# Optimization experiments

Hardware: AMD Instinct MI355X
Metric: run time of the kernel (lower is better)

Reference implementation:

```python
import jax, jax.numpy as jnp
import numpy as np

B, N, D = 8, 4096, 512
H, RANK = 8, 64
HD = D // H


def _xavier(key, shape):
    fan_out, fan_in = shape
    limit = (6.0 / (fan_in + fan_out)) ** 0.5
    return jax.random.uniform(key, shape, jnp.float32, -limit, limit)


def setup_inputs() -> dict:
    key = jax.random.key(0)
    ks = jax.random.split(key, 10)
    return {
        "x": jax.random.normal(ks[0], (B, N, D), jnp.float32),
        "graph_bias": jax.random.normal(ks[1], (N, N), jnp.float32),
        # torch nn.Linear weight convention: (out_features, in_features)
        "w_qd": _xavier(ks[2], (RANK, D)),
        "w_qu": _xavier(ks[3], (D, RANK)),
        "w_kd": _xavier(ks[4], (RANK, D)),
        "w_ku": _xavier(ks[5], (D, RANK)),
        "w_vd": _xavier(ks[6], (RANK, D)),
        "w_vu": _xavier(ks[7], (D, RANK)),
        "w_od": _xavier(ks[8], (RANK, D)),
        "w_ou": _xavier(ks[9], (D, RANK)),
    }


def _feature_map(x):
    # ELU + 1 (ensures non-negativity for linear attention)
    return jax.nn.elu(x) + 1.0


def _heads(t):
    # (B, N, D) -> (B, H, N, HD)
    return t.reshape(B, N, H, HD).transpose(0, 2, 1, 3)


def reference(x, graph_bias, w_qd, w_qu, w_kd, w_ku, w_vd, w_vu, w_od, w_ou):
    # low-rank QKV projections (Linear has no bias): x @ W_down.T @ W_up.T
    Q = (x @ w_qd.T) @ w_qu.T
    K = (x @ w_kd.T) @ w_ku.T
    V = (x @ w_vd.T) @ w_vu.T
    Q = _feature_map(_heads(Q))
    K = _feature_map(_heads(K))
    V = _heads(V)

    # linear attention: phi(Q) (phi(K)^T V), O(N)
    KV = jnp.einsum('bhnd,bhnD->bhdD', K, V)
    out = jnp.einsum('bhnd,bhdD->bhnD', Q, KV)
    K_sum = K.sum(axis=2)                                   # (B,H,HD)
    normalizer = jnp.einsum('bhnd,bhd->bhn', Q, K_sum)      # (B,H,N)
    normalizer = jnp.clip(normalizer, 1e-6, None)
    out = out / normalizer[..., None]

    # graph-bias branch: dense softmax attention over learned structure
    bias_attn = jax.nn.softmax(graph_bias, axis=-1)         # (N,N)
    V_flat = V.transpose(0, 2, 1, 3).reshape(B, N, D)
    bias_out = jnp.einsum('ij,bjd->bid', bias_attn, V_flat)
    bias_out = _heads(bias_out)
    out = out + 0.1 * bias_out

    out = out.transpose(0, 2, 1, 3).reshape(B, N, D)
    out = (out @ w_od.T) @ w_ou.T
    return out
```

## Files before the change

kernel.cpp:

```cpp
#include <hip/hip_runtime.h>

typedef unsigned short u16;
typedef __attribute__((ext_vector_type(8))) short short8;
typedef __attribute__((ext_vector_type(4))) float f32x4;

#define GLD16(g, l) __builtin_amdgcn_global_load_lds((const __attribute__((address_space(1))) void*)(g), (__attribute__((address_space(3))) void*)(l), 16, 0, 0)

__device__ __forceinline__ u16 f2bf(float f){
  unsigned x = __float_as_uint(f);
  return (u16)((x + 0x7FFFu + ((x >> 16) & 1u)) >> 16);
}
__device__ __forceinline__ float bf2f(u16 u){
  return __uint_as_float(((unsigned)u) << 16);
}

__global__ __launch_bounds__(256) void castf2b(const float* __restrict__ src, u16* __restrict__ dst){
  const size_t i = ((size_t)blockIdx.x * 256 + threadIdx.x) * 8;
  float4 a = *reinterpret_cast<const float4*>(src + i);
  float4 b = *reinterpret_cast<const float4*>(src + i + 4);
  ushort4 o0 = {f2bf(a.x), f2bf(a.y), f2bf(a.z), f2bf(a.w)};
  ushort4 o1 = {f2bf(b.x), f2bf(b.y), f2bf(b.z), f2bf(b.w)};
  *reinterpret_cast<ushort4*>(dst + i) = o0;
  *reinterpret_cast<ushort4*>(dst + i + 4) = o1;
}

__global__ __launch_bounds__(256) void cast_pad(const float* __restrict__ src, u16* __restrict__ dst){
  const int i = blockIdx.x * 256 + threadIdx.x;
  const int e = i * 8;
  const int r = e >> 9;
  ushort4 o0 = {0,0,0,0}, o1 = {0,0,0,0};
  if(r < 64){
    float4 a = *reinterpret_cast<const float4*>(src + e);
    float4 b = *reinterpret_cast<const float4*>(src + e + 4);
    o0 = ushort4{f2bf(a.x), f2bf(a.y), f2bf(a.z), f2bf(a.w)};
    o1 = ushort4{f2bf(b.x), f2bf(b.y), f2bf(b.z), f2bf(b.w)};
  }
  *reinterpret_cast<ushort4*>(dst + e) = o0;
  *reinterpret_cast<ushort4*>(dst + e + 4) = o1;
}

__global__ __launch_bounds__(256) void softmax_rows(const float* __restrict__ gb,
                                                    u16* __restrict__ attn){
  const int row = blockIdx.x;
  const float* rp = gb + (size_t)row * 4096;
  u16* op = attn + (size_t)row * 4096;
  const int t = threadIdx.x;
  float4 v[4];
  float mx = -3.4e38f;
#pragma unroll
  for(int k = 0; k < 4; k++){
    v[k] = *reinterpret_cast<const float4*>(rp + k*1024 + t*4);
    mx = fmaxf(mx, fmaxf(fmaxf(v[k].x, v[k].y), fmaxf(v[k].z, v[k].w)));
  }
#pragma unroll
  for(int off = 32; off > 0; off >>= 1) mx = fmaxf(mx, __shfl_xor(mx, off, 64));
  __shared__ float sred[4];
  __shared__ float sred2[4];
  const int wid = t >> 6, lane = t & 63;
  if(lane == 0) sred[wid] = mx;
  __syncthreads();
  mx = fmaxf(fmaxf(sred[0], sred[1]), fmaxf(sred[2], sred[3]));
  float s = 0.f;
#pragma unroll
  for(int k = 0; k < 4; k++){
    v[k].x = __expf(v[k].x - mx); v[k].y = __expf(v[k].y - mx);
    v[k].z = __expf(v[k].z - mx); v[k].w = __expf(v[k].w - mx);
    s += v[k].x + v[k].y + v[k].z + v[k].w;
  }
#pragma unroll
  for(int off = 32; off > 0; off >>= 1) s += __shfl_xor(s, off, 64);
  if(lane == 0) sred2[wid] = s;
  __syncthreads();
  s = sred2[0] + sred2[1] + sred2[2] + sred2[3];
  const float inv = 1.f / s;
#pragma unroll
  for(int k = 0; k < 4; k++){
    ushort4 o;
    o.x = f2bf(v[k].x * inv); o.y = f2bf(v[k].y * inv);
    o.z = f2bf(v[k].z * inv); o.w = f2bf(v[k].w * inv);
    *reinterpret_cast<ushort4*>(op + k*1024 + t*4) = o;
  }
}

__global__ __launch_bounds__(256) void combine_w(const float* __restrict__ wu,
                                                 const float* __restrict__ wd,
                                                 u16* __restrict__ dst){
  __shared__ float au[64][68];
  __shared__ float bd[64][68];
  const int t = threadIdx.x;
  const int o0 = blockIdx.x << 6, i0 = blockIdx.y << 6;
#pragma unroll
  for(int q = 0; q < 4; q++){
    const int row = (q << 4) + (t >> 4);
    const int c4  = (t & 15) << 2;
    float4 u = *reinterpret_cast<const float4*>(wu + (size_t)(o0 + row) * 64 + c4);
    au[c4+0][row] = u.x; au[c4+1][row] = u.y; au[c4+2][row] = u.z; au[c4+3][row] = u.w;
    float4 v = *reinterpret_cast<const float4*>(wd + (size_t)row * 512 + i0 + c4);
    bd[row][c4+0] = v.x; bd[row][c4+1] = v.y; bd[row][c4+2] = v.z; bd[row][c4+3] = v.w;
  }
  __syncthreads();
  const int tr = t >> 4, tc = t & 15;
  float acc[4][4] = {};
#pragma unroll
  for(int kk = 0; kk < 64; kk++){
    const float4 a4 = *reinterpret_cast<const float4*>(&au[kk][tr << 2]);
    const float4 b4 = *reinterpret_cast<const float4*>(&bd[kk][tc << 2]);
    const float av_[4] = {a4.x, a4.y, a4.z, a4.w};
    const float bv_[4] = {b4.x, b4.y, b4.z, b4.w};
#pragma unroll
    for(int i = 0; i < 4; i++)
#pragma unroll
      for(int j = 0; j < 4; j++) acc[i][j] = fmaf(av_[i], bv_[j], acc[i][j]);
  }
#pragma unroll
  for(int i = 0; i < 4; i++){
    ushort4 o;
    o.x = f2bf(acc[i][0]); o.y = f2bf(acc[i][1]); o.z = f2bf(acc[i][2]); o.w = f2bf(acc[i][3]);
    *reinterpret_cast<ushort4*>(dst + (size_t)(o0 + (tr << 2) + i) * 512 + i0 + (tc << 2)) = o;
  }
}

__global__ __launch_bounds__(256) void wvo_kernel(const float* __restrict__ w_od,
                                                  const float* __restrict__ w_vu,
                                                  float* __restrict__ Wvo){
  __shared__ float As[16][68];
  __shared__ float Bs[16][68];
  const int t = threadIdx.x;
  const int tr = t >> 4, tc = t & 15;
  float acc[4][4] = {};
  for(int k0 = 0; k0 < 512; k0 += 16){
    __syncthreads();
#pragma unroll
    for(int q = 0; q < 4; q++){
      const int idx = q * 256 + t;
      const int kk = idx >> 6, l = idx & 63;
      As[kk][l] = w_od[(size_t)l * 512 + k0 + kk];
      Bs[kk][l] = w_vu[(size_t)(k0 + kk) * 64 + l];
    }
    __syncthreads();
#pragma unroll
    for(int kk = 0; kk < 16; kk++){
      const float4 a4 = *reinterpret_cast<const float4*>(&As[kk][tr << 2]);
      const float4 b4 = *reinterpret_cast<const float4*>(&Bs[kk][tc << 2]);
      const float av_[4] = {a4.x, a4.y, a4.z, a4.w};
      const float bv_[4] = {b4.x, b4.y, b4.z, b4.w};
#pragma unroll
      for(int i = 0; i < 4; i++)
#pragma unroll
        for(int j = 0; j < 4; j++) acc[i][j] = fmaf(av_[i], bv_[j], acc[i][j]);
    }
  }
#pragma unroll
  for(int i = 0; i < 4; i++)
#pragma unroll
    for(int j = 0; j < 4; j++)
      Wvo[(size_t)((tr << 2) + i) * 64 + (tc << 2) + j] = 0.1f * acc[i][j];
}

__global__ __launch_bounds__(256) void qkvlow_gemm(const u16* __restrict__ Am, const u16* __restrict__ Bm,
                                                   u16* __restrict__ Qt, u16* __restrict__ Kt,
                                                   u16* __restrict__ Vlowt, float* __restrict__ Ksum){
  __shared__ u16 As[128 * 32];
  __shared__ u16 Bs[128 * 32];
  const int t = threadIdx.x;
  const int wid = t >> 6, lane = t & 63;
  const int wr = wid >> 1, wc = wid & 1;
  const int bm = blockIdx.x << 7, bn = blockIdx.y << 7;
  f32x4 acc[4][4];
#pragma unroll
  for(int m = 0; m < 4; m++)
#pragma unroll
    for(int n = 0; n < 4; n++) acc[m][n] = f32x4{0.f, 0.f, 0.f, 0.f};
  const int frow = lane & 15;
  const int kg8  = (lane >> 4) << 3;
  const int c0 = t, c1 = t + 256;
  for(int k0 = 0; k0 < 512; k0 += 32){
    GLD16(Am + (size_t)(bm + (c0 >> 2)) * 512 + k0 + ((c0 & 3) << 3), ((char*)As) + (wid << 10));
    GLD16(Am + (size_t)(bm + (c1 >> 2)) * 512 + k0 + ((c1 & 3) << 3), ((char*)As) + 4096 + (wid << 10));
    GLD16(Bm + (size_t)(bn + (c0 >> 2)) * 512 + k0 + ((c0 & 3) << 3), ((char*)Bs) + (wid << 10));
    GLD16(Bm + (size_t)(bn + (c1 >> 2)) * 512 + k0 + ((c1 & 3) << 3), ((char*)Bs) + 4096 + (wid << 10));
    __syncthreads();
    short8 af[4], bfr[4];
#pragma unroll
    for(int m = 0; m < 4; m++){
      af[m]  = *reinterpret_cast<const short8*>(As + (((wr << 6) + (m << 4) + frow) << 5) + kg8);
      bfr[m] = *reinterpret_cast<const short8*>(Bs + (((wc << 6) + (m << 4) + frow) << 5) + kg8);
    }
#pragma unroll
    for(int m = 0; m < 4; m++)
#pragma unroll
      for(int n = 0; n < 4; n++)
        acc[m][n] = __builtin_amdgcn_mfma_f32_16x16x32_bf16(af[m], bfr[n], acc[m][n], 0, 0, 0);
    __syncthreads();
  }
  const int cn = lane & 15, rb4 = (lane >> 4) << 2;
  const int b = bm >> 12;
#pragma unroll
  for(int nf = 0; nf < 4; nf++){
    const int col = bn + (wc << 6) + (nf << 4) + cn;
    u16* rowp;
    bool isK = false, isQorK = false;
    if(col < 512){
      rowp = Qt + ((((size_t)((b << 3) + (col >> 6)) << 6) + (col & 63)) << 12);
      isQorK = true;
    } else if(col < 1024){
      const int c = col - 512;
      rowp = Kt + ((((size_t)((b << 3) + (c >> 6)) << 6) + (c & 63)) << 12);
      isK = true; isQorK = true;
    } else {
      const int j = col - 1024;
      if(j >= 64) continue;
      rowp = Vlowt + ((size_t)((b << 6) + j) << 12);
    }
    float ks = 0.f;
#pragma unroll
    for(int mf = 0; mf < 4; mf++){
      const int nn0 = (bm & 4095) + (wr << 6) + (mf << 4) + rb4;
      float v0 = acc[mf][nf][0], v1 = acc[mf][nf][1], v2 = acc[mf][nf][2], v3 = acc[mf][nf][3];
      if(isQorK){
        v0 = v0 > 0.f ? v0 + 1.f : __expf(v0);
        v1 = v1 > 0.f ? v1 + 1.f : __expf(v1);
        v2 = v2 > 0.f ? v2 + 1.f : __expf(v2);
        v3 = v3 > 0.f ? v3 + 1.f : __expf(v3);
      }
      if(isK) ks += v0 + v1 + v2 + v3;
      ushort4 o = {f2bf(v0), f2bf(v1), f2bf(v2), f2bf(v3)};
      *reinterpret_cast<ushort4*>(rowp + nn0) = o;
    }
    if(isK){
      ks += __shfl_xor(ks, 16);
      ks += __shfl_xor(ks, 32);
      if(lane < 16){
        const int c = col - 512;
        atomicAdd(Ksum + ((size_t)((b << 3) + (c >> 6)) << 6) + (c & 63), ks);
      }
    }
  }
}

__global__ __launch_bounds__(256) void kvlow_gemm(const u16* __restrict__ Kt,
                                                  const u16* __restrict__ Vlowt,
                                                  float* __restrict__ KVlow){
  __shared__ u16 As[64 * 32];
  __shared__ u16 Bs[64 * 32];
  const int bh = blockIdx.x, sp = blockIdx.y;
  const int b = bh >> 3;
  const int t = threadIdx.x;
  const int wid = t >> 6, lane = t & 63;
  const int frow = lane & 15, kg8 = (lane >> 4) << 3;
  const size_t kbase = (size_t)bh << 18;
  const size_t vbase = (size_t)b << 18;
  const int srow = t >> 2, soff = (t & 3) << 3;
  f32x4 acc[4];
#pragma unroll
  for(int n = 0; n < 4; n++) acc[n] = f32x4{0.f, 0.f, 0.f, 0.f};
  const int nend = (sp << 10) + 1024;
  for(int n0 = sp << 10; n0 < nend; n0 += 32){
    GLD16(Kt    + kbase + ((size_t)srow << 12) + n0 + soff, ((char*)As) + (wid << 10));
    GLD16(Vlowt + vbase + ((size_t)srow << 12) + n0 + soff, ((char*)Bs) + (wid << 10));
    __syncthreads();
    short8 af = *reinterpret_cast<const short8*>(As + (((wid << 4) + frow) << 5) + kg8);
#pragma unroll
    for(int n = 0; n < 4; n++){
      short8 bf8 = *reinterpret_cast<const short8*>(Bs + (((n << 4) + frow) << 5) + kg8);
      acc[n] = __builtin_amdgcn_mfma_f32_16x16x32_bf16(af, bf8, acc[n], 0, 0, 0);
    }
    __syncthreads();
  }
  const int cn = lane & 15, rb4 = (lane >> 4) << 2;
#pragma unroll
  for(int n = 0; n < 4; n++)
#pragma unroll
    for(int j = 0; j < 4; j++){
      const int d = (wid << 4) + rb4 + j;
      const int jj = (n << 4) + cn;
      atomicAdd(KVlow + ((size_t)bh << 12) + (size_t)d * 64 + jj, acc[n][j]);
    }
}

__global__ __launch_bounds__(256) void kv_apply(const float* __restrict__ KVlow,
                                                const float* __restrict__ w_vu,
                                                float* __restrict__ KVt){
  __shared__ float Kl[64][68];
  __shared__ float Wl[64][68];
  const int bh = blockIdx.x, h = bh & 7;
  const int t = threadIdx.x;
#pragma unroll
  for(int q = 0; q < 4; q++){
    const int row = (q << 4) + (t >> 4);
    const int c4  = (t & 15) << 2;
    float4 v = *reinterpret_cast<const float4*>(KVlow + ((size_t)bh << 12) + (size_t)row * 64 + c4);
    Kl[c4+0][row] = v.x; Kl[c4+1][row] = v.y; Kl[c4+2][row] = v.z; Kl[c4+3][row] = v.w;
    float4 w = *reinterpret_cast<const float4*>(w_vu + (size_t)((h << 6) + row) * 64 + c4);
    Wl[c4+0][row] = w.x; Wl[c4+1][row] = w.y; Wl[c4+2][row] = w.z; Wl[c4+3][row] = w.w;
  }
  __syncthreads();
  const int tr = t >> 4, tc = t & 15;
  float acc[4][4] = {};
#pragma unroll
  for(int kk = 0; kk < 64; kk++){
    const float4 a4 = *reinterpret_cast<const float4*>(&Wl[kk][tr << 2]);
    const float4 b4 = *reinterpret_cast<const float4*>(&Kl[kk][tc << 2]);
    const float av_[4] = {a4.x, a4.y, a4.z, a4.w};
    const float bv_[4] = {b4.x, b4.y, b4.z, b4.w};
#pragma unroll
    for(int i = 0; i < 4; i++)
#pragma unroll
      for(int j = 0; j < 4; j++) acc[i][j] = fmaf(av_[i], bv_[j], acc[i][j]);
  }
#pragma unroll
  for(int i = 0; i < 4; i++){
    float4 o = {acc[i][0], acc[i][1], acc[i][2], acc[i][3]};
    *reinterpret_cast<float4*>(KVt + ((size_t)bh << 12) + (size_t)((tr << 2) + i) * 64 + (tc << 2)) = o;
  }
}

__global__ __launch_bounds__(256) void bias_pv(const u16* __restrict__ Am,
                                               const u16* __restrict__ Bm,
                                               float* __restrict__ Pv){
  __shared__ u16 As[128 * 32];
  __shared__ u16 Bs[128 * 32];
  const int t = threadIdx.x;
  const int wid = t >> 6, lane = t & 63;
  const int wr = wid >> 1, wc = wid & 1;
  const int bm = blockIdx.x << 7, bn = blockIdx.y << 7, kz = blockIdx.z;
  f32x4 acc[4][4];
#pragma unroll
  for(int m = 0; m < 4; m++)
#pragma unroll
    for(int n = 0; n < 4; n++) acc[m][n] = f32x4{0.f, 0.f, 0.f, 0.f};
  const int frow = lane & 15;
  const int kg8  = (lane >> 4) << 3;
  const int c0 = t, c1 = t + 256;
  const int kend = (kz << 11) + 2048;
  for(int k0 = kz << 11; k0 < kend; k0 += 32){
    GLD16(Am + ((size_t)(bm + (c0 >> 2)) << 12) + k0 + ((c0 & 3) << 3), ((char*)As) + (wid << 10));
    GLD16(Am + ((size_t)(bm + (c1 >> 2)) << 12) + k0 + ((c1 & 3) << 3), ((char*)As) + 4096 + (wid << 10));
    GLD16(Bm + ((size_t)(bn + (c0 >> 2)) << 12) + k0 + ((c0 & 3) << 3), ((char*)Bs) + (wid << 10));
    GLD16(Bm + ((size_t)(bn + (c1 >> 2)) << 12) + k0 + ((c1 & 3) << 3), ((char*)Bs) + 4096 + (wid << 10));
    __syncthreads();
    short8 af[4], bfr[4];
#pragma unroll
    for(int m = 0; m < 4; m++){
      af[m]  = *reinterpret_cast<const short8*>(As + (((wr << 6) + (m << 4) + frow) << 5) + kg8);
      bfr[m] = *reinterpret_cast<const short8*>(Bs + (((wc << 6) + (m << 4) + frow) << 5) + kg8);
    }
#pragma unroll
    for(int m = 0; m < 4; m++)
#pragma unroll
      for(int n = 0; n < 4; n++)
        acc[m][n] = __builtin_amdgcn_mfma_f32_16x16x32_bf16(af[m], bfr[n], acc[m][n], 0, 0, 0);
    __syncthreads();
  }
  const int cn = lane & 15, rb4 = (lane >> 4) << 2;
  float* P = Pv + (size_t)kz * 2097152;
#pragma unroll
  for(int m = 0; m < 4; m++){
    const int row0 = bm + (wr << 6) + (m << 4) + rb4;
#pragma unroll
    for(int n = 0; n < 4; n++){
      const int col = bn + (wc << 6) + (n << 4) + cn;
#pragma unroll
      for(int j = 0; j < 4; j++)
        P[(size_t)(row0 + j) * 512 + col] = acc[m][n][j];
    }
  }
}

__global__ __launch_bounds__(256) void linattn(const u16* __restrict__ Qt,
                                               const float* __restrict__ KVt,
                                               const float* __restrict__ Ksum,
                                               u16* __restrict__ midb){
  __shared__ float qs[64][64];
  __shared__ float kvs[64][64];
  __shared__ float nrm[64];
  __shared__ float ksl[64];
  const int nblk = blockIdx.x, bhi = blockIdx.y;
  const int b = bhi >> 3, h = bhi & 7;
  const int n0 = nblk << 6;
  const int t = threadIdx.x;
#pragma unroll
  for(int q = 0; q < 4; q++){
    const int row = (q << 4) + (t >> 4);
    const int c4  = (t & 15) << 2;
    ushort4 u = *reinterpret_cast<const ushort4*>(Qt + ((((size_t)bhi << 6) + row) << 12) + n0 + c4);
    qs[row][c4+0] = bf2f(u.x); qs[row][c4+1] = bf2f(u.y); qs[row][c4+2] = bf2f(u.z); qs[row][c4+3] = bf2f(u.w);
    float4 v = *reinterpret_cast<const float4*>(KVt + ((size_t)bhi << 12) + (row << 6) + c4);
    kvs[c4+0][row] = v.x; kvs[c4+1][row] = v.y; kvs[c4+2][row] = v.z; kvs[c4+3][row] = v.w;
  }
  if(t < 64) ksl[t] = Ksum[((size_t)bhi << 6) + t];
  __syncthreads();
  if(t < 64){
    float s = 0.f;
    for(int d = 0; d < 64; d++) s = fmaf(qs[d][t], ksl[d], s);
    nrm[t] = fmaxf(s, 1e-6f);
  }
  __syncthreads();
  const int tr = t >> 4, tc = t & 15;
  float acc[4][4] = {};
#pragma unroll
  for(int kk = 0; kk < 64; kk++){
    const float4 a4 = *reinterpret_cast<const float4*>(&qs[kk][tr << 2]);
    const float4 b4 = *reinterpret_cast<const float4*>(&kvs[kk][tc << 2]);
    const float av_[4] = {a4.x, a4.y, a4.z, a4.w};
    const float bv_[4] = {b4.x, b4.y, b4.z, b4.w};
#pragma unroll
    for(int i = 0; i < 4; i++)
#pragma unroll
      for(int j = 0; j < 4; j++) acc[i][j] = fmaf(av_[i], bv_[j], acc[i][j]);
  }
#pragma unroll
  for(int i = 0; i < 4; i++){
    const int gn = n0 + (tr << 2) + i;
    const float inv = 1.f / nrm[(tr << 2) + i];
    const size_t oi = (((size_t)b << 12) + gn) * 512 + h * 64 + (tc << 2);
    ushort4 o = {f2bf(acc[i][0] * inv), f2bf(acc[i][1] * inv),
                 f2bf(acc[i][2] * inv), f2bf(acc[i][3] * inv)};
    *reinterpret_cast<ushort4*>(midb + oi) = o;
  }
}

__global__ __launch_bounds__(256) void biaslow(const float* __restrict__ Pv,
                                               const float* __restrict__ Wvo,
                                               float* __restrict__ G){
  __shared__ float Pl[64][68];
  __shared__ float Wl[64][68];
  const int nt = blockIdx.x, b = blockIdx.y;
  const int n0 = nt << 6;
  const int t = threadIdx.x;
#pragma unroll
  for(int q = 0; q < 4; q++){
    const int row = (q << 4) + (t >> 4);
    const int c4  = (t & 15) << 2;
    float4 v  = *reinterpret_cast<const float4*>(Pv + (size_t)(n0 + row) * 512 + (b << 6) + c4);
    float4 v2 = *reinterpret_cast<const float4*>(Pv + 2097152 + (size_t)(n0 + row) * 512 + (b << 6) + c4);
    Pl[c4+0][row] = v.x + v2.x; Pl[c4+1][row] = v.y + v2.y;
    Pl[c4+2][row] = v.z + v2.z; Pl[c4+3][row] = v.w + v2.w;
    float4 w = *reinterpret_cast<const float4*>(Wvo + (size_t)row * 64 + c4);
    Wl[c4+0][row] = w.x; Wl[c4+1][row] = w.y; Wl[c4+2][row] = w.z; Wl[c4+3][row] = w.w;
  }
  __syncthreads();
  const int tr = t >> 4, tc = t & 15;
  float acc[4][4] = {};
#pragma unroll
  for(int kk = 0; kk < 64; kk++){
    const float4 a4 = *reinterpret_cast<const float4*>(&Pl[kk][tr << 2]);
    const float4 b4 = *reinterpret_cast<const float4*>(&Wl[kk][tc << 2]);
    const float av_[4] = {a4.x, a4.y, a4.z, a4.w};
    const float bv_[4] = {b4.x, b4.y, b4.z, b4.w};
#pragma unroll
    for(int i = 0; i < 4; i++)
#pragma unroll
      for(int j = 0; j < 4; j++) acc[i][j] = fmaf(av_[i], bv_[j], acc[i][j]);
  }
#pragma unroll
  for(int i = 0; i < 4; i++){
    float4 o = {acc[i][0], acc[i][1], acc[i][2], acc[i][3]};
    *reinterpret_cast<float4*>(G + (size_t)(((size_t)b << 12) + n0 + (tr << 2) + i) * 64 + (tc << 2)) = o;
  }
}

__global__ __launch_bounds__(256) void down_gemm(const u16* __restrict__ Am,
                                                 const u16* __restrict__ Bw,
                                                 const float* __restrict__ Gin,
                                                 u16* __restrict__ Gb){
  __shared__ u16 As[128 * 32];
  const int t = threadIdx.x;
  const int wid = t >> 6, lane = t & 63;
  const int bm = blockIdx.x << 7;
  const int frow = lane & 15, kg8 = (lane >> 4) << 3;
  f32x4 acc[2][4];
#pragma unroll
  for(int m = 0; m < 2; m++)
#pragma unroll
    for(int n = 0; n < 4; n++) acc[m][n] = f32x4{0.f, 0.f, 0.f, 0.f};
  const int c0 = t, c1 = t + 256;
  for(int k0 = 0; k0 < 512; k0 += 32){
    GLD16(Am + (size_t)(bm + (c0 >> 2)) * 512 + k0 + ((c0 & 3) << 3), ((char*)As) + (wid << 10));
    GLD16(Am + (size_t)(bm + (c1 >> 2)) * 512 + k0 + ((c1 & 3) << 3), ((char*)As) + 4096 + (wid << 10));
    __syncthreads();
    short8 af[2], bfr[4];
#pragma unroll
    for(int m = 0; m < 2; m++)
      af[m] = *reinterpret_cast<const short8*>(As + (((wid << 5) + (m << 4) + frow) << 5) + kg8);
#pragma unroll
    for(int n = 0; n < 4; n++)
      bfr[n] = *reinterpret_cast<const short8*>(Bw + (size_t)((n << 4) + frow) * 512 + k0 + kg8);
#pragma unroll
    for(int m = 0; m < 2; m++)
#pragma unroll
      for(int n = 0; n < 4; n++)
        acc[m][n] = __builtin_amdgcn_mfma_f32_16x16x32_bf16(af[m], bfr[n], acc[m][n], 0, 0, 0);
    __syncthreads();
  }
  const int cn = lane & 15, rb4 = (lane >> 4) << 2;
#pragma unroll
  for(int m = 0; m < 2; m++){
#pragma unroll
    for(int n = 0; n < 4; n++){
      const int col = (n << 4) + cn;
#pragma unroll
      for(int j = 0; j < 4; j++){
        const int r = bm + (wid << 5) + (m << 4) + rb4 + j;
        const float v = acc[m][n][j] + Gin[(size_t)r * 64 + col];
        Gb[(size_t)r * 64 + col] = f2bf(v);
      }
    }
  }
}

__global__ __launch_bounds__(256) void up_gemm(const u16* __restrict__ Am,
                                               const u16* __restrict__ Bw,
                                               float* __restrict__ C){
  const int t = threadIdx.x;
  const int wid = t >> 6, lane = t & 63;
  const int wr = wid >> 1, wc = wid & 1;
  const int bm = blockIdx.x << 7, bn = blockIdx.y << 7;
  const int frow = lane & 15, kg8 = (lane >> 4) << 3;
  f32x4 acc[4][4];
#pragma unroll
  for(int m = 0; m < 4; m++)
#pragma unroll
    for(int n = 0; n < 4; n++) acc[m][n] = f32x4{0.f, 0.f, 0.f, 0.f};
  short8 af[4][2], bfr[4][2];
#pragma unroll
  for(int m = 0; m < 4; m++)
#pragma unroll
    for(int kk = 0; kk < 2; kk++)
      af[m][kk] = *reinterpret_cast<const short8*>(Am + (size_t)(bm + (wr << 6) + (m << 4) + frow) * 64 + (kk << 5) + kg8);
#pragma unroll
  for(int n = 0; n < 4; n++)
#pragma unroll
    for(int kk = 0; kk < 2; kk++)
      bfr[n][kk] = *reinterpret_cast<const short8*>(Bw + (size_t)(bn + (wc << 6) + (n << 4) + frow) * 64 + (kk << 5) + kg8);
#pragma unroll
  for(int m = 0; m < 4; m++)
#pragma unroll
    for(int n = 0; n < 4; n++){
      acc[m][n] = __builtin_amdgcn_mfma_f32_16x16x32_bf16(af[m][0], bfr[n][0], acc[m][n], 0, 0, 0);
      acc[m][n] = __builtin_amdgcn_mfma_f32_16x16x32_bf16(af[m][1], bfr[n][1], acc[m][n], 0, 0, 0);
    }
  const int cn = lane & 15, rb4 = (lane >> 4) << 2;
#pragma unroll
  for(int m = 0; m < 4; m++){
    const int row0 = bm + (wr << 6) + (m << 4) + rb4;
#pragma unroll
    for(int n = 0; n < 4; n++){
      const int col = bn + (wc << 6) + (n << 4) + cn;
#pragma unroll
      for(int j = 0; j < 4; j++)
        C[(size_t)(row0 + j) * 512 + col] = acc[m][n][j];
    }
  }
}

extern "C" void kernel_launch(void* const* d_in, const int* in_sizes, int n_in,
                              void* d_out, int out_size, void* d_ws, size_t ws_size,
                              hipStream_t stream){
  const float* x    = (const float*)d_in[0];
  const float* gb   = (const float*)d_in[1];
  const float* w_qd = (const float*)d_in[2];
  const float* w_qu = (const float*)d_in[3];
  const float* w_kd = (const float*)d_in[4];
  const float* w_ku = (const float*)d_in[5];
  const float* w_vd = (const float*)d_in[6];
  const float* w_vu = (const float*)d_in[7];
  const float* w_od = (const float*)d_in[8];
  const float* w_ou = (const float*)d_in[9];
  float* out = (float*)d_out;
  char* ws = (char*)d_ws;

  u16*   xb    = (u16*)  (ws);
  u16*   Kt    = (u16*)  (ws + 33554432);
  u16*   Wall  = (u16*)  (ws + 67108864);
  u16*   wodb  = (u16*)  (ws + 68288512);
  u16*   woub  = (u16*)  (ws + 68354048);
  float* Wvo   = (float*)(ws + 68419584);
  u16*   Qt    = (u16*)  (ws + 68435968);
  u16*   Vlowt = (u16*)  (ws + 101990400);
  u16*   attn  = (u16*)  (ws + 106184704);
  float* Pv    = (float*)(ws + 139739136);
  float* KVlow = (float*)(ws + 156516352);
  float* KVt   = (float*)(ws + 157564928);
  float* Ksum  = (float*)(ws + 158613504);
  u16*   midb  = (u16*)  (ws);
  float* G     = (float*)(ws + 33554432);
  u16*   Gb    = (u16*)  (ws + 41943040);

  hipMemsetAsync(KVlow, 0, 2113536, stream);

  combine_w<<<dim3(8, 8), 256, 0, stream>>>(w_qu, w_qd, Wall);
  combine_w<<<dim3(8, 8), 256, 0, stream>>>(w_ku, w_kd, Wall + 262144);
  cast_pad<<<32, 256, 0, stream>>>(w_vd, Wall + 524288);
  castf2b<<<16, 256, 0, stream>>>(w_od, wodb);
  castf2b<<<16, 256, 0, stream>>>(w_ou, woub);
  wvo_kernel<<<1, 256, 0, stream>>>(w_od, w_vu, Wvo);

  castf2b<<<8192, 256, 0, stream>>>(x, xb);
  softmax_rows<<<4096, 256, 0, stream>>>(gb, attn);

  qkvlow_gemm<<<dim3(256, 9), 256, 0, stream>>>(xb, Wall, Qt, Kt, Vlowt, Ksum);

  kvlow_gemm<<<dim3(64, 4), 256, 0, stream>>>(Kt, Vlowt, KVlow);
  kv_apply<<<64, 256, 0, stream>>>(KVlow, w_vu, KVt);

  bias_pv<<<dim3(32, 4, 2), 256, 0, stream>>>(attn, Vlowt, Pv);

  linattn<<<dim3(64, 64), 256, 0, stream>>>(Qt, KVt, Ksum, midb);

  biaslow<<<dim3(64, 8), 256, 0, stream>>>(Pv, Wvo, G);

  down_gemm<<<256, 256, 0, stream>>>(midb, wodb, G, Gb);

  up_gemm<<<dim3(256, 4), 256, 0, stream>>>(Gb, woub, out);
}
```

Before: 473.0 us.

## Double-buffer LDS tiles in GEMM kernels and merge weight-cast launches

Four GEMM kernels (qkvlow, kvlow, bias_pv, down) now use two LDS buffers. Each iteration issues the async global-to-LDS load for the next k-tile before running the MFMAs on the current one, so only one barrier per step remains instead of two. Three small weight-cast kernels are also merged into a single prep_w launch to cut launch overhead. The price is twice the shared memory per block, which may lower occupancy.

```diff
diff --git a/kernel.cpp b/kernel.cpp
--- a/kernel.cpp
+++ b/kernel.cpp
@@ -12,6 +12,45 @@
 }
 __device__ __forceinline__ float bf2f(u16 u){
   return __uint_as_float(((unsigned)u) << 16);
+}
+
+__global__ __launch_bounds__(256) void prep_w(const float* __restrict__ w_od,
+                                              const float* __restrict__ w_ou,
+                                              const float* __restrict__ w_vd,
+                                              u16* __restrict__ wodb,
+                                              u16* __restrict__ woub,
+                                              u16* __restrict__ wpad){
+  const int bid = blockIdx.x, t = threadIdx.x;
+  if(bid < 16){
+    const size_t i = ((size_t)bid * 256 + t) * 8;
+    float4 a = *reinterpret_cast<const float4*>(w_od + i);
+    float4 b = *reinterpret_cast<const float4*>(w_od + i + 4);
+    ushort4 o0 = {f2bf(a.x), f2bf(a.y), f2bf(a.z), f2bf(a.w)};
+    ushort4 o1 = {f2bf(b.x), f2bf(b.y), f2bf(b.z), f2bf(b.w)};
+    *reinterpret_cast<ushort4*>(wodb + i) = o0;
+    *reinterpret_cast<ushort4*>(wodb + i + 4) = o1;
+  } else if(bid < 32){
+    const size_t i = ((size_t)(bid - 16) * 256 + t) * 8;
+    float4 a = *reinterpret_cast<const float4*>(w_ou + i);
+    float4 b = *reinterpret_cast<const float4*>(w_ou + i + 4);
+    ushort4 o0 = {f2bf(a.x), f2bf(a.y), f2bf(a.z), f2bf(a.w)};
+    ushort4 o1 = {f2bf(b.x), f2bf(b.y), f2bf(b.z), f2bf(b.w)};
+    *reinterpret_cast<ushort4*>(woub + i) = o0;
+    *reinterpret_cast<ushort4*>(woub + i + 4) = o1;
+  } else {
+    const int i = (bid - 32) * 256 + t;
+    const int e = i * 8;
+    const int r = e >> 9;
+    ushort4 o0 = {0,0,0,0}, o1 = {0,0,0,0};
+    if(r < 64){
+      float4 a = *reinterpret_cast<const float4*>(w_vd + e);
+      float4 b = *reinterpret_cast<const float4*>(w_vd + e + 4);
+      o0 = ushort4{f2bf(a.x), f2bf(a.y), f2bf(a.z), f2bf(a.w)};
+      o1 = ushort4{f2bf(b.x), f2bf(b.y), f2bf(b.z), f2bf(b.w)};
+    }
+    *reinterpret_cast<ushort4*>(wpad + e) = o0;
+    *reinterpret_cast<ushort4*>(wpad + e + 4) = o1;
+  }
 }
 
 __global__ __launch_bounds__(256) void castf2b(const float* __restrict__ src, u16* __restrict__ dst){
@@ -24,21 +63,6 @@
   *reinterpret_cast<ushort4*>(dst + i + 4) = o1;
 }
 
-__global__ __launch_bounds__(256) void cast_pad(const float* __restrict__ src, u16* __restrict__ dst){
-  const int i = blockIdx.x * 256 + threadIdx.x;
-  const int e = i * 8;
-  const int r = e >> 9;
-  ushort4 o0 = {0,0,0,0}, o1 = {0,0,0,0};
-  if(r < 64){
-    float4 a = *reinterpret_cast<const float4*>(src + e);
-    float4 b = *reinterpret_cast<const float4*>(src + e + 4);
-    o0 = ushort4{f2bf(a.x), f2bf(a.y), f2bf(a.z), f2bf(a.w)};
-    o1 = ushort4{f2bf(b.x), f2bf(b.y), f2bf(b.z), f2bf(b.w)};
-  }
-  *reinterpret_cast<ushort4*>(dst + e) = o0;
-  *reinterpret_cast<ushort4*>(dst + e + 4) = o1;
-}
-
 __global__ __launch_bounds__(256) void softmax_rows(const float* __restrict__ gb,
                                                     u16* __restrict__ attn){
   const int row = blockIdx.x;
@@ -160,8 +184,8 @@
 __global__ __launch_bounds__(256) void qkvlow_gemm(const u16* __restrict__ Am, const u16* __restrict__ Bm,
                                                    u16* __restrict__ Qt, u16* __restrict__ Kt,
                                                    u16* __restrict__ Vlowt, float* __restrict__ Ksum){
-  __shared__ u16 As[128 * 32];
-  __shared__ u16 Bs[128 * 32];
+  __shared__ u16 As[2][4096];
+  __shared__ u16 Bs[2][4096];
   const int t = threadIdx.x;
   const int wid = t >> 6, lane = t & 63;
   const int wr = wid >> 1, wc = wid & 1;
@@ -174,25 +198,36 @@
   const int frow = lane & 15;
   const int kg8  = (lane >> 4) << 3;
   const int c0 = t, c1 = t + 256;
-  for(int k0 = 0; k0 < 512; k0 += 32){
-    GLD16(Am + (size_t)(bm + (c0 >> 2)) * 512 + k0 + ((c0 & 3) << 3), ((char*)As) + (wid << 10));
-    GLD16(Am + (size_t)(bm + (c1 >> 2)) * 512 + k0 + ((c1 & 3) << 3), ((char*)As) + 4096 + (wid << 10));
-    GLD16(Bm + (size_t)(bn + (c0 >> 2)) * 512 + k0 + ((c0 & 3) << 3), ((char*)Bs) + (wid << 10));
-    GLD16(Bm + (size_t)(bn + (c1 >> 2)) * 512 + k0 + ((c1 & 3) << 3), ((char*)Bs) + 4096 + (wid << 10));
+  const size_t a0 = (size_t)(bm + (c0 >> 2)) * 512 + ((c0 & 3) << 3);
+  const size_t a1 = (size_t)(bm + (c1 >> 2)) * 512 + ((c1 & 3) << 3);
+  const size_t b0 = (size_t)(bn + (c0 >> 2)) * 512 + ((c0 & 3) << 3);
+  const size_t b1 = (size_t)(bn + (c1 >> 2)) * 512 + ((c1 & 3) << 3);
+#define QSTAGE(bf, k0) do{ \
+    GLD16(Am + a0 + (k0), ((char*)&As[bf][0]) + (wid << 10)); \
+    GLD16(Am + a1 + (k0), ((char*)&As[bf][0]) + 4096 + (wid << 10)); \
+    GLD16(Bm + b0 + (k0), ((char*)&Bs[bf][0]) + (wid << 10)); \
+    GLD16(Bm + b1 + (k0), ((char*)&Bs[bf][0]) + 4096 + (wid << 10)); }while(0)
+#define QCOMP(bf) do{ \
+    short8 af[4], bfr[4]; \
+    _Pragma("unroll") \
+    for(int m = 0; m < 4; m++){ \
+      af[m]  = *reinterpret_cast<const short8*>(&As[bf][(((wr << 6) + (m << 4) + frow) << 5) + kg8]); \
+      bfr[m] = *reinterpret_cast<const short8*>(&Bs[bf][(((wc << 6) + (m << 4) + frow) << 5) + kg8]); } \
+    _Pragma("unroll") \
+    for(int m = 0; m < 4; m++) \
+      _Pragma("unroll") \
+      for(int n = 0; n < 4; n++) \
+        acc[m][n] = __builtin_amdgcn_mfma_f32_16x16x32_bf16(af[m], bfr[n], acc[m][n], 0, 0, 0); }while(0)
+  QSTAGE(0, 0);
+  __syncthreads();
+  int cur = 0;
+  for(int k0 = 32; k0 < 512; k0 += 32){
+    QSTAGE(cur ^ 1, k0);
+    QCOMP(cur);
     __syncthreads();
-    short8 af[4], bfr[4];
-#pragma unroll
-    for(int m = 0; m < 4; m++){
-      af[m]  = *reinterpret_cast<const short8*>(As + (((wr << 6) + (m << 4) + frow) << 5) + kg8);
-      bfr[m] = *reinterpret_cast<const short8*>(Bs + (((wc << 6) + (m << 4) + frow) << 5) + kg8);
-    }
-#pragma unroll
-    for(int m = 0; m < 4; m++)
-#pragma unroll
-      for(int n = 0; n < 4; n++)
-        acc[m][n] = __builtin_amdgcn_mfma_f32_16x16x32_bf16(af[m], bfr[n], acc[m][n], 0, 0, 0);
-    __syncthreads();
-  }
+    cur ^= 1;
+  }
+  QCOMP(cur);
   const int cn = lane & 15, rb4 = (lane >> 4) << 2;
   const int b = bm >> 12;
 #pragma unroll
@@ -236,13 +271,15 @@
       }
     }
   }
+#undef QSTAGE
+#undef QCOMP
 }
 
 __global__ __launch_bounds__(256) void kvlow_gemm(const u16* __restrict__ Kt,
                                                   const u16* __restrict__ Vlowt,
                                                   float* __restrict__ KVlow){
-  __shared__ u16 As[64 * 32];
-  __shared__ u16 Bs[64 * 32];
+  __shared__ u16 As[2][2048];
+  __shared__ u16 Bs[2][2048];
   const int bh = blockIdx.x, sp = blockIdx.y;
   const int b = bh >> 3;
   const int t = threadIdx.x;
@@ -251,22 +288,31 @@
   const size_t kbase = (size_t)bh << 18;
   const size_t vbase = (size_t)b << 18;
   const int srow = t >> 2, soff = (t & 3) << 3;
+  const size_t asrc = kbase + ((size_t)srow << 12) + soff;
+  const size_t bsrc = vbase + ((size_t)srow << 12) + soff;
   f32x4 acc[4];
 #pragma unroll
   for(int n = 0; n < 4; n++) acc[n] = f32x4{0.f, 0.f, 0.f, 0.f};
-  const int nend = (sp << 10) + 1024;
-  for(int n0 = sp << 10; n0 < nend; n0 += 32){
-    GLD16(Kt    + kbase + ((size_t)srow << 12) + n0 + soff, ((char*)As) + (wid << 10));
-    GLD16(Vlowt + vbase + ((size_t)srow << 12) + n0 + soff, ((char*)Bs) + (wid << 10));
+#define KSTAGE(bf, n0) do{ \
+    GLD16(Kt    + asrc + (n0), ((char*)&As[bf][0]) + (wid << 10)); \
+    GLD16(Vlowt + bsrc + (n0), ((char*)&Bs[bf][0]) + (wid << 10)); }while(0)
+#define KCOMP(bf) do{ \
+    short8 af = *reinterpret_cast<const short8*>(&As[bf][(((wid << 4) + frow) << 5) + kg8]); \
+    _Pragma("unroll") \
+    for(int n = 0; n < 4; n++){ \
+      short8 bf8 = *reinterpret_cast<const short8*>(&Bs[bf][(((n << 4) + frow) << 5) + kg8]); \
+      acc[n] = __builtin_amdgcn_mfma_f32_16x16x32_bf16(af, bf8, acc[n], 0, 0, 0); } }while(0)
+  const int nbeg = sp << 10;
+  KSTAGE(0, nbeg);
+  __syncthreads();
+  int cur = 0;
+  for(int n0 = nbeg + 32; n0 < nbeg + 1024; n0 += 32){
+    KSTAGE(cur ^ 1, n0);
+    KCOMP(cur);
     __syncthreads();
-    short8 af = *reinterpret_cast<const short8*>(As + (((wid << 4) + frow) << 5) + kg8);
-#pragma unroll
-    for(int n = 0; n < 4; n++){
-      short8 bf8 = *reinterpret_cast<const short8*>(Bs + (((n << 4) + frow) << 5) + kg8);
-      acc[n] = __builtin_amdgcn_mfma_f32_16x16x32_bf16(af, bf8, acc[n], 0, 0, 0);
-    }
-    __syncthreads();
-  }
+    cur ^= 1;
+  }
+  KCOMP(cur);
   const int cn = lane & 15, rb4 = (lane >> 4) << 2;
 #pragma unroll
   for(int n = 0; n < 4; n++)
@@ -276,6 +322,8 @@
       const int jj = (n << 4) + cn;
       atomicAdd(KVlow + ((size_t)bh << 12) + (size_t)d * 64 + jj, acc[n][j]);
     }
+#undef KSTAGE
+#undef KCOMP
 }
 
 __global__ __launch_bounds__(256) void kv_apply(const float* __restrict__ KVlow,
@@ -318,8 +366,8 @@
 __global__ __launch_bounds__(256) void bias_pv(const u16* __restrict__ Am,
                                                const u16* __restrict__ Bm,
                                                float* __restrict__ Pv){
-  __shared__ u16 As[128 * 32];
-  __shared__ u16 Bs[128 * 32];
+  __shared__ u16 As[2][4096];
+  __shared__ u16 Bs[2][4096];
   const int t = threadIdx.x;
   const int wid = t >> 6, lane = t & 63;
   const int wr = wid >> 1, wc = wid & 1;
@@ -332,26 +380,37 @@
   const int frow = lane & 15;
   const int kg8  = (lane >> 4) << 3;
   const int c0 = t, c1 = t + 256;
-  const int kend = (kz << 11) + 2048;
-  for(int k0 = kz << 11; k0 < kend; k0 += 32){
-    GLD16(Am + ((size_t)(bm + (c0 >> 2)) << 12) + k0 + ((c0 & 3) << 3), ((char*)As) + (wid << 10));
-    GLD16(Am + ((size_t)(bm + (c1 >> 2)) << 12) + k0 + ((c1 & 3) << 3), ((char*)As) + 4096 + (wid << 10));
-    GLD16(Bm + ((size_t)(bn + (c0 >> 2)) << 12) + k0 + ((c0 & 3) << 3), ((char*)Bs) + (wid << 10));
-    GLD16(Bm + ((size_t)(bn + (c1 >> 2)) << 12) + k0 + ((c1 & 3) << 3), ((char*)Bs) + 4096 + (wid << 10));
+  const size_t a0 = ((size_t)(bm + (c0 >> 2)) << 12) + ((c0 & 3) << 3);
+  const size_t a1 = ((size_t)(bm + (c1 >> 2)) << 12) + ((c1 & 3) << 3);
+  const size_t b0 = ((size_t)(bn + (c0 >> 2)) << 12) + ((c0 & 3) << 3);
+  const size_t b1 = ((size_t)(bn + (c1 >> 2)) << 12) + ((c1 & 3) << 3);
+#define PSTAGE(bf, k0) do{ \
+    GLD16(Am + a0 + (k0), ((char*)&As[bf][0]) + (wid << 10)); \
+    GLD16(Am + a1 + (k0), ((char*)&As[bf][0]) + 4096 + (wid << 10)); \
+    GLD16(Bm + b0 + (k0), ((char*)&Bs[bf][0]) + (wid << 10)); \
+    GLD16(Bm + b1 + (k0), ((char*)&Bs[bf][0]) + 4096 + (wid << 10)); }while(0)
+#define PCOMP(bf) do{ \
+    short8 af[4], bfr[4]; \
+    _Pragma("unroll") \
+    for(int m = 0; m < 4; m++){ \
+      af[m]  = *reinterpret_cast<const short8*>(&As[bf][(((wr << 6) + (m << 4) + frow) << 5) + kg8]); \
+      bfr[m] = *reinterpret_cast<const short8*>(&Bs[bf][(((wc << 6) + (m << 4) + frow) << 5) + kg8]); } \
+    _Pragma("unroll") \
+    for(int m = 0; m < 4; m++) \
+      _Pragma("unroll") \
+      for(int n = 0; n < 4; n++) \
+        acc[m][n] = __builtin_amdgcn_mfma_f32_16x16x32_bf16(af[m], bfr[n], acc[m][n], 0, 0, 0); }while(0)
+  const int kbeg = kz << 11;
+  PSTAGE(0, kbeg);
+  __syncthreads();
+  int cur = 0;
+  for(int k0 = kbeg + 32; k0 < kbeg + 2048; k0 += 32){
+    PSTAGE(cur ^ 1, k0);
+    PCOMP(cur);
     __syncthreads();
-    short8 af[4], bfr[4];
-#pragma unroll
-    for(int m = 0; m < 4; m++){
-      af[m]  = *reinterpret_cast<const short8*>(As + (((wr << 6) + (m << 4) + frow) << 5) + kg8);
-      bfr[m] = *reinterpret_cast<const short8*>(Bs + (((wc << 6) + (m << 4) + frow) << 5) + kg8);
-    }
-#pragma unroll
-    for(int m = 0; m < 4; m++)
-#pragma unroll
-      for(int n = 0; n < 4; n++)
-        acc[m][n] = __builtin_amdgcn_mfma_f32_16x16x32_bf16(af[m], bfr[n], acc[m][n], 0, 0, 0);
-    __syncthreads();
-  }
+    cur ^= 1;
+  }
+  PCOMP(cur);
   const int cn = lane & 15, rb4 = (lane >> 4) << 2;
   float* P = Pv + (size_t)kz * 2097152;
 #pragma unroll
@@ -365,6 +424,8 @@
         P[(size_t)(row0 + j) * 512 + col] = acc[m][n][j];
     }
   }
+#undef PSTAGE
+#undef PCOMP
 }
 
 __global__ __launch_bounds__(256) void linattn(const u16* __restrict__ Qt,
@@ -464,7 +525,7 @@
                                                  const u16* __restrict__ Bw,
                                                  const float* __restrict__ Gin,
                                                  u16* __restrict__ Gb){
-  __shared__ u16 As[128 * 32];
+  __shared__ u16 As[2][4096];
   const int t = threadIdx.x;
   const int wid = t >> 6, lane = t & 63;
   const int bm = blockIdx.x << 7;
@@ -475,24 +536,34 @@
 #pragma unroll
     for(int n = 0; n < 4; n++) acc[m][n] = f32x4{0.f, 0.f, 0.f, 0.f};
   const int c0 = t, c1 = t + 256;
-  for(int k0 = 0; k0 < 512; k0 += 32){
-    GLD16(Am + (size_t)(bm + (c0 >> 2)) * 512 + k0 + ((c0 & 3) << 3), ((char*)As) + (wid << 10));
-    GLD16(Am + (size_t)(bm + (c1 >> 2)) * 512 + k0 + ((c1 & 3) << 3), ((char*)As) + 4096 + (wid << 10));
+  const size_t a0 = (size_t)(bm + (c0 >> 2)) * 512 + ((c0 & 3) << 3);
+  const size_t a1 = (size_t)(bm + (c1 >> 2)) * 512 + ((c1 & 3) << 3);
+#define DSTAGE(bf, k0) do{ \
+    GLD16(Am + a0 + (k0), ((char*)&As[bf][0]) + (wid << 10)); \
+    GLD16(Am + a1 + (k0), ((char*)&As[bf][0]) + 4096 + (wid << 10)); }while(0)
+#define DCOMP(bf, k0) do{ \
+    short8 af[2], bfr[4]; \
+    _Pragma("unroll") \
+    for(int m = 0; m < 2; m++) \
+      af[m] = *reinterpret_cast<const short8*>(&As[bf][(((wid << 5) + (m << 4) + frow) << 5) + kg8]); \
+    _Pragma("unroll") \
+    for(int n = 0; n < 4; n++) \
+      bfr[n] = *reinterpret_cast<const short8*>(Bw + (size_t)((n << 4) + frow) * 512 + (k0) + kg8); \
+    _Pragma("unroll") \
+    for(int m = 0; m < 2; m++) \
+      _Pragma("unroll") \
+      for(int n = 0; n < 4; n++) \
+        acc[m][n] = __builtin_amdgcn_mfma_f32_16x16x32_bf16(af[m], bfr[n], acc[m][n], 0, 0, 0); }while(0)
+  DSTAGE(0, 0);
+  __syncthreads();
+  int cur = 0;
+  for(int k0 = 32; k0 < 512; k0 += 32){
+    DSTAGE(cur ^ 1, k0);
+    DCOMP(cur, k0 - 32);
     __syncthreads();
-    short8 af[2], bfr[4];
-#pragma unroll
-    for(int m = 0; m < 2; m++)
-      af[m] = *reinterpret_cast<const short8*>(As + (((wid << 5) + (m << 4) + frow) << 5) + kg8);
-#pragma unroll
-    for(int n = 0; n < 4; n++)
-      bfr[n] = *reinterpret_cast<const short8*>(Bw + (size_t)((n << 4) + frow) * 512 + k0 + kg8);
-#pragma unroll
-    for(int m = 0; m < 2; m++)
-#pragma unroll
-      for(int n = 0; n < 4; n++)
-        acc[m][n] = __builtin_amdgcn_mfma_f32_16x16x32_bf16(af[m], bfr[n], acc[m][n], 0, 0, 0);
-    __syncthreads();
-  }
+    cur ^= 1;
+  }
+  DCOMP(cur, 480);
   const int cn = lane & 15, rb4 = (lane >> 4) << 2;
 #pragma unroll
   for(int m = 0; m < 2; m++){
@@ -507,6 +578,8 @@
       }
     }
   }
+#undef DSTAGE
+#undef DCOMP
 }
 
 __global__ __launch_bounds__(256) void up_gemm(const u16* __restrict__ Am,
@@ -591,10 +664,8 @@
 
   combine_w<<<dim3(8, 8), 256, 0, stream>>>(w_qu, w_qd, Wall);
   combine_w<<<dim3(8, 8), 256, 0, stream>>>(w_ku, w_kd, Wall + 262144);
-  cast_pad<<<32, 256, 0, stream>>>(w_vd, Wall + 524288);
-  castf2b<<<16, 256, 0, stream>>>(w_od, wodb);
-  castf2b<<<16, 256, 0, stream>>>(w_ou, woub);
   wvo_kernel<<<1, 256, 0, stream>>>(w_od, w_vu, Wvo);
+  prep_w<<<64, 256, 0, stream>>>(w_od, w_ou, w_vd, wodb, woub, Wall + 524288);
 
   castf2b<<<8192, 256, 0, stream>>>(x, xb);
   softmax_rows<<<4096, 256, 0, stream>>>(gb, attn);
```

Measured after the change: 452.7 us. 4.3% less time.
